# Kernel tuning notes

Measured on AMD Instinct MI355X. Metric: run time of the kernel, lower is better.

## Reference

```python
import jax, jax.numpy as jnp
import numpy as np

EPS = 1e-08
SINKHORN_ITERS = 5
SINKHORN_TAU = 0.05


def l2_normalize(x, axis=-1):
    return x / (jnp.linalg.norm(x, axis=axis, keepdims=True) + EPS)


def sinkhorn_balanced(logits, iters=SINKHORN_ITERS, tau=SINKHORN_TAU):
    # logits: [B, N, K]
    b, n, k = logits.shape
    q = jnp.exp(logits / tau)
    q = q / (jnp.sum(q, axis=(1, 2), keepdims=True) + EPS)
    target_row = 1.0 / float(n)
    target_col = 1.0 / float(k)
    for _ in range(iters):
        q = q / (jnp.sum(q, axis=2, keepdims=True) + EPS) * target_row
        q = q / (jnp.sum(q, axis=1, keepdims=True) + EPS) * target_col
    q = q / (jnp.sum(q, axis=2, keepdims=True) + EPS)
    return q


def assign(x, proto):
    x_n = l2_normalize(x)          # [B,N,D]
    p_n = l2_normalize(proto)      # [K,D]
    sim = jnp.einsum('bnd,kd->bnk', x_n, p_n)
    a = sinkhorn_balanced(sim)
    z_rec = jnp.einsum('bnk,kd->bnd', a, p_n)
    return z_rec, a, sim


def setup_inputs() -> dict:
    key = jax.random.key(0)
    k1, k2, k3, k4 = jax.random.split(key, 4)
    B, N, D, K = 16, 1024, 256, 256
    return {
        'f_rgb': jax.random.normal(k1, (B, N, D), dtype=jnp.float32),
        'f_sn': jax.random.normal(k2, (B, N, D), dtype=jnp.float32),
        'proto_rgb': jax.random.normal(k3, (K, D), dtype=jnp.float32) * 0.02,
        'proto_sn': jax.random.normal(k4, (K, D), dtype=jnp.float32) * 0.02,
    }


def reference(f_rgb, f_sn, proto_rgb, proto_sn):
    z_rgb, assign_rgb, sim_rgb = assign(f_rgb, proto_rgb)
    z_sn, assign_sn, sim_sn = assign(f_sn, proto_sn)
    # cross-modal consistency maps: [B,N,N]
    rgb_to_sn = jnp.matmul(assign_rgb, jnp.swapaxes(assign_sn, -1, -2))
    sn_to_rgb = jnp.matmul(assign_sn, jnp.swapaxes(assign_rgb, -1, -2))
    sem_consistency = 0.5 * (
        1.0 - jnp.clip(jnp.mean(rgb_to_sn), 0.0, 1.0)
        + 1.0 - jnp.clip(jnp.mean(sn_to_rgb), 0.0, 1.0)
    )
    return (z_rgb, z_sn, assign_rgb, assign_sn, sim_rgb, sim_sn, sem_consistency)
```

## Files before the change

kernel.cpp:

```cpp
#include <hip/hip_runtime.h>
#include <hip/hip_bf16.h>
#include <cstdint>
#include <cstddef>

#define EPS 1e-8f

typedef __attribute__((ext_vector_type(8))) short short8;
typedef __attribute__((ext_vector_type(4))) float floatx4;

static constexpr int Bb = 16, Nn = 1024, Dd = 256, Kk = 256;
static constexpr int M = Bb * Nn;
static constexpr size_t PM = (size_t)M * 256;

static constexpr size_t OUT_Z      = 0;
static constexpr size_t OUT_ASSIGN = 2 * PM;
static constexpr size_t OUT_SIM    = 4 * PM;
static constexpr size_t OUT_SEM    = 6 * PM;

static constexpr size_t OFF_QB  = 16777216;
static constexpr size_t OFF_PN  = 33554432;
static constexpr size_t OFF_PNT = 33816576;
static constexpr size_t OFF_U   = 34078720;
static constexpr size_t OFF_T   = 34209792;
static constexpr size_t OFF_SC  = 34209920;
static constexpr size_t OFF_CS  = 34406528;
static constexpr size_t ZERO_OFF = OFF_T;
static constexpr size_t ZERO_SZ  = 128 + 196608 + 32768;
static constexpr int    NZ_FLOATS = (int)(ZERO_SZ / 4);

__device__ __forceinline__ unsigned short f2bf(float f) {
    unsigned int b = __float_as_uint(f);
    b += 0x7fffu + ((b >> 16) & 1u);
    return (unsigned short)(b >> 16);
}
__device__ __forceinline__ float bf2f(unsigned short u) {
    return __uint_as_float(((unsigned int)u) << 16);
}

typedef const __attribute__((address_space(1))) unsigned int* gas_u32p;
typedef __attribute__((address_space(3))) unsigned int* las_u32p;
__device__ __forceinline__ void lds_cp16(const unsigned short* g, short* l) {
    __builtin_amdgcn_global_load_lds((gas_u32p)g, (las_u32p)l, 16, 0, 0);
}

__global__ __launch_bounds__(64) void proto_kernel(const float* __restrict__ pr,
                                                   const float* __restrict__ ps,
                                                   unsigned short* __restrict__ pn,
                                                   unsigned short* __restrict__ pnt,
                                                   float* __restrict__ zp) {
    int gid = blockIdx.x * 64 + threadIdx.x;
    for (int i = gid; i < NZ_FLOATS; i += 32768) zp[i] = 0.f;

    int row = blockIdx.x & 255;
    int mod = blockIdx.x >> 8;
    const float* p = (mod ? ps : pr) + (size_t)row * 256;
    int lane = threadIdx.x;
    float4 v = ((const float4*)p)[lane];
    float ss = v.x * v.x + v.y * v.y + v.z * v.z + v.w * v.w;
    #pragma unroll
    for (int m = 1; m < 64; m <<= 1) ss += __shfl_xor(ss, m);
    float sc = 1.0f / (sqrtf(ss) + EPS);
    ushort4 u4;
    u4.x = f2bf(v.x * sc); u4.y = f2bf(v.y * sc);
    u4.z = f2bf(v.z * sc); u4.w = f2bf(v.w * sc);
    *(ushort4*)(pn + (size_t)mod * 65536 + (size_t)row * 256 + lane * 4) = u4;
    unsigned short* pt = pnt + (size_t)mod * 65536 + row;
    pt[(size_t)(lane * 4 + 0) * 256] = u4.x;
    pt[(size_t)(lane * 4 + 1) * 256] = u4.y;
    pt[(size_t)(lane * 4 + 2) * 256] = u4.z;
    pt[(size_t)(lane * 4 + 3) * 256] = u4.w;
}

__global__ __launch_bounds__(256) void gemm0_fused(const float* __restrict__ fr,
                                                   const float* __restrict__ fs,
                                                   const unsigned short* __restrict__ pn,
                                                   unsigned short* __restrict__ qb,
                                                   float* __restrict__ doutf,
                                                   float* __restrict__ Tg) {
    __shared__ __align__(16) char smem[81920];
    short* Afull = (short*)smem;
    short* Bl    = (short*)(smem + 65536);

    int bx = blockIdx.x, by = blockIdx.y, mod = blockIdx.z;
    int t = threadIdx.x, lane = t & 63, wv = t >> 6;
    int wrow = (wv >> 1) * 64, wcol = (wv & 1) * 64;
    int g = lane >> 4, ml = lane & 15;

    const float* F0 = (mod ? fs : fr) + (size_t)by * 128 * 256;
    const unsigned short* B0 = pn + (size_t)mod * 65536 + (size_t)bx * 128 * 256;

    for (int bs = 0; bs < 4; bs++) {
        int rbase = wv * 32 + bs * 8;
        float4 vv[8];
        #pragma unroll
        for (int i = 0; i < 8; i++)
            vv[i] = ((const float4*)(F0 + (size_t)(rbase + i) * 256))[lane];
        #pragma unroll
        for (int i = 0; i < 8; i++) {
            float ss = vv[i].x * vv[i].x + vv[i].y * vv[i].y
                     + vv[i].z * vv[i].z + vv[i].w * vv[i].w;
            #pragma unroll
            for (int m = 1; m < 64; m <<= 1) ss += __shfl_xor(ss, m);
            float sc = 1.0f / (sqrtf(ss) + EPS);
            ushort4 u4;
            u4.x = f2bf(vv[i].x * sc); u4.y = f2bf(vv[i].y * sc);
            u4.z = f2bf(vv[i].z * sc); u4.w = f2bf(vv[i].w * sc);
            int row = rbase + i;
            int off = row * 256 + (((lane >> 1) ^ (row & 7)) << 3) + ((lane & 1) << 2);
            *(ushort4*)&Afull[off] = u4;
        }
    }

    floatx4 acc[4][4];
    #pragma unroll
    for (int i = 0; i < 4; i++)
        #pragma unroll
        for (int j = 0; j < 4; j++) acc[i][j] = (floatx4){0.f, 0.f, 0.f, 0.f};

    for (int kh = 0; kh < 4; kh++) {
        #pragma unroll
        for (int i = 0; i < 4; i++) {
            int sI = i * 256 + t;
            int r = sI >> 3, cs = sI & 7;
            int cg = cs ^ (r & 7);
            size_t goff = (size_t)r * 256 + kh * 64 + cg * 8;
            lds_cp16(B0 + goff, &Bl[sI * 8]);
        }
        __syncthreads();
        #pragma unroll
        for (int ks = 0; ks < 2; ks++) {
            short8 af[4], bfr[4];
            int c = ks * 4 + g;
            int c8 = kh * 8 + c;
            #pragma unroll
            for (int mt = 0; mt < 4; mt++) {
                int row = wrow + mt * 16 + ml;
                af[mt] = *(const short8*)&Afull[row * 256 + ((c8 ^ (row & 7)) << 3)];
            }
            #pragma unroll
            for (int nt = 0; nt < 4; nt++) {
                int col = wcol + nt * 16 + ml;
                bfr[nt] = *(const short8*)&Bl[col * 64 + ((c ^ (col & 7)) << 3)];
            }
            #pragma unroll
            for (int mt = 0; mt < 4; mt++)
                #pragma unroll
                for (int nt = 0; nt < 4; nt++)
                    acc[mt][nt] = __builtin_amdgcn_mfma_f32_16x16x32_bf16(af[mt], bfr[nt], acc[mt][nt], 0, 0, 0);
        }
        __syncthreads();
    }

    int g4 = g << 2;
    float tsum = 0.f;
    #pragma unroll
    for (int mt = 0; mt < 4; mt++)
        #pragma unroll
        for (int nt = 0; nt < 4; nt++)
            #pragma unroll
            for (int reg = 0; reg < 4; reg++) {
                float s = acc[mt][nt][reg];
                int row = by * 128 + wrow + mt * 16 + g4 + reg;
                int col = bx * 128 + wcol + nt * 16 + ml;
                size_t idx = (size_t)row * 256 + col;
                doutf[OUT_SIM + (size_t)mod * PM + idx] = s;
                unsigned short eb = f2bf(__expf(s * 20.0f));
                qb[(size_t)mod * PM + idx] = eb;
                tsum += bf2f(eb);
            }
    #pragma unroll
    for (int mk = 1; mk < 64; mk <<= 1) tsum += __shfl_xor(tsum, mk);
    float* tred = (float*)(smem + 65536);
    if (lane == 0) tred[wv] = tsum;
    __syncthreads();
    if (t == 0) atomicAdd(&Tg[mod * 16 + (by >> 3)], tred[0] + tred[1] + tred[2] + tred[3]);
}

__global__ __launch_bounds__(256) void pass_kernel(const unsigned short* __restrict__ qbg,
                                                   float* __restrict__ u,
                                                   const float* __restrict__ Tg,
                                                   float* __restrict__ Sc,
                                                   int pass) {
    __shared__ float vcur[256];
    __shared__ float unl[32];
    __shared__ float wsum[4][256];
    int tile = blockIdx.x, b = blockIdx.y, mod = blockIdx.z;
    int t = threadIdx.x;
    {
        float v = 1.0f;
        for (int j = 1; j < pass; j++) {
            float sc = Sc[((size_t)(mod * 6 + j) * 16 + b) * 256 + t];
            v = v * (1.0f / 256.0f) / (v * sc + EPS);
        }
        vcur[t] = v;
    }
    __syncthreads();

    int r = t >> 3, q = t & 7;
    size_t row = (size_t)b * 1024 + tile * 32 + r;
    const unsigned short* qrow = qbg + ((size_t)mod * M + row) * 256;
    const short8* q8 = (const short8*)(qrow + q * 32);
    const float4* v4 = (const float4*)(vcur + q * 32);
    float sr = 0.f;
    #pragma unroll
    for (int i = 0; i < 4; i++) {
        short8 qv = q8[i];
        float4 va = v4[2 * i], vb = v4[2 * i + 1];
        sr += bf2f((unsigned short)qv[0]) * va.x + bf2f((unsigned short)qv[1]) * va.y
            + bf2f((unsigned short)qv[2]) * va.z + bf2f((unsigned short)qv[3]) * va.w
            + bf2f((unsigned short)qv[4]) * vb.x + bf2f((unsigned short)qv[5]) * vb.y
            + bf2f((unsigned short)qv[6]) * vb.z + bf2f((unsigned short)qv[7]) * vb.w;
    }
    sr += __shfl_xor(sr, 1);
    sr += __shfl_xor(sr, 2);
    sr += __shfl_xor(sr, 4);

    float up = (pass == 1) ? 1.0f / (Tg[mod * 16 + b] + EPS) : u[(size_t)mod * M + row];
    float un = up * (1.0f / 1024.0f) / (up * sr + EPS);
    if (q == 0) {
        u[(size_t)mod * M + row] = un;
        unl[r] = un;
    }
    __syncthreads();

    int wv = t >> 6, lane = t & 63;
    float c0 = 0.f, c1 = 0.f, c2 = 0.f, c3 = 0.f;
    size_t rowbase = (size_t)mod * M + (size_t)b * 1024 + tile * 32;
    #pragma unroll
    for (int rr8 = 0; rr8 < 8; rr8++) {
        int rr = wv * 8 + rr8;
        float unr = unl[rr];
        ushort4 qv = *(const ushort4*)(qbg + (rowbase + rr) * 256 + lane * 4);
        c0 += bf2f(qv.x) * unr;
        c1 += bf2f(qv.y) * unr;
        c2 += bf2f(qv.z) * unr;
        c3 += bf2f(qv.w) * unr;
    }
    *(float4*)&wsum[wv][lane * 4] = make_float4(c0, c1, c2, c3);
    __syncthreads();
    {
        float ssum = wsum[0][t] + wsum[1][t] + wsum[2][t] + wsum[3][t];
        atomicAdd(&Sc[((size_t)(mod * 6 + pass) * 16 + b) * 256 + t], ssum);
    }
}

__global__ __launch_bounds__(256) void gemm1_fused(const unsigned short* __restrict__ qbg,
                                                   const unsigned short* __restrict__ pnt,
                                                   const float* __restrict__ u,
                                                   const float* __restrict__ Sc,
                                                   float* __restrict__ cs,
                                                   float* __restrict__ doutf) {
    __shared__ __align__(16) char smem[81920];
    short* Afull = (short*)smem;
    short* Bl    = (short*)(smem + 65536);
    float* vl    = (float*)(smem + 65536);
    float* unl   = (float*)(smem + 65536 + 1024);
    float* wsum  = (float*)(smem + 65536 + 2048);

    int bx = blockIdx.x, by = blockIdx.y, mod = blockIdx.z;
    int b = by >> 3;
    int t = threadIdx.x, lane = t & 63, wv = t >> 6;
    int wrow = (wv >> 1) * 64, wcol = (wv & 1) * 64;
    int g = lane >> 4, ml = lane & 15;
    int r = t >> 3, q = t & 7;
    size_t rowg0 = (size_t)by * 128;

    if (t < 256) {
        float v = 1.0f;
        #pragma unroll
        for (int j = 1; j <= 5; j++) {
            float scv = Sc[((size_t)(mod * 6 + j) * 16 + b) * 256 + t];
            v = v * (1.0f / 256.0f) / (v * scv + EPS);
        }
        vl[t] = v;
    }
    __syncthreads();

    const float* vb0 = vl + q * 32;
    for (int s = 0; s < 4; s++) {
        int rl = s * 32 + r;
        size_t rowg = rowg0 + rl;
        const short8* q8 = (const short8*)(qbg + ((size_t)mod * PM + rowg * 256) + q * 32);
        float sr = 0.f;
        #pragma unroll
        for (int i = 0; i < 4; i++) {
            short8 qv = q8[i];
            float4 va = *(const float4*)(vb0 + i * 8);
            float4 vb = *(const float4*)(vb0 + i * 8 + 4);
            sr += bf2f((unsigned short)qv[0]) * va.x + bf2f((unsigned short)qv[1]) * va.y
                + bf2f((unsigned short)qv[2]) * va.z + bf2f((unsigned short)qv[3]) * va.w
                + bf2f((unsigned short)qv[4]) * vb.x + bf2f((unsigned short)qv[5]) * vb.y
                + bf2f((unsigned short)qv[6]) * vb.z + bf2f((unsigned short)qv[7]) * vb.w;
        }
        sr += __shfl_xor(sr, 1);
        sr += __shfl_xor(sr, 2);
        sr += __shfl_xor(sr, 4);
        float up = u[(size_t)mod * M + rowg];
        float un = up / (up * sr + EPS);
        if (q == 0) unl[rl] = un;
    }
    __syncthreads();

    {
        float c0 = 0.f, c1 = 0.f, c2 = 0.f, c3 = 0.f;
        float4 vv = *(const float4*)(vl + lane * 4);
        float* aout = doutf + OUT_ASSIGN + (size_t)mod * PM;
        for (int s = 0; s < 4; s++) {
            #pragma unroll
            for (int k = 0; k < 8; k++) {
                int rl = s * 32 + wv * 8 + k;
                size_t rowg = rowg0 + rl;
                float unr = unl[rl];
                ushort4 qv = *(const ushort4*)(qbg + ((size_t)mod * PM + rowg * 256) + lane * 4);
                float4 a = make_float4(bf2f(qv.x) * unr * vv.x, bf2f(qv.y) * unr * vv.y,
                                       bf2f(qv.z) * unr * vv.z, bf2f(qv.w) * unr * vv.w);
                if (bx == 0) *(float4*)(aout + rowg * 256 + lane * 4) = a;
                ushort4 o;
                o.x = f2bf(a.x); o.y = f2bf(a.y); o.z = f2bf(a.z); o.w = f2bf(a.w);
                int off = rl * 256 + (((lane >> 1) ^ (rl & 7)) << 3) + ((lane & 1) << 2);
                *(ushort4*)&Afull[off] = o;
                c0 += a.x; c1 += a.y; c2 += a.z; c3 += a.w;
            }
        }
        *(float4*)&wsum[wv * 256 + lane * 4] = make_float4(c0, c1, c2, c3);
    }
    __syncthreads();
    if (bx == 0 && t < 256) {
        float ssum = wsum[0 * 256 + t] + wsum[1 * 256 + t] + wsum[2 * 256 + t] + wsum[3 * 256 + t];
        atomicAdd(&cs[((size_t)mod * 16 + b) * 256 + t], ssum);
    }
    __syncthreads();

    const unsigned short* B0 = pnt + (size_t)mod * 65536 + (size_t)bx * 128 * 256;
    floatx4 acc[4][4];
    #pragma unroll
    for (int i = 0; i < 4; i++)
        #pragma unroll
        for (int j = 0; j < 4; j++) acc[i][j] = (floatx4){0.f, 0.f, 0.f, 0.f};

    for (int kh = 0; kh < 4; kh++) {
        #pragma unroll
        for (int i = 0; i < 4; i++) {
            int sI = i * 256 + t;
            int rr = sI >> 3, cc = sI & 7;
            int cg = cc ^ (rr & 7);
            size_t goff = (size_t)rr * 256 + kh * 64 + cg * 8;
            lds_cp16(B0 + goff, &Bl[sI * 8]);
        }
        __syncthreads();
        #pragma unroll
        for (int ks = 0; ks < 2; ks++) {
            short8 af[4], bfr[4];
            int c = ks * 4 + g;
            int c8 = kh * 8 + c;
            #pragma unroll
            for (int mt = 0; mt < 4; mt++) {
                int row = wrow + mt * 16 + ml;
                af[mt] = *(const short8*)&Afull[row * 256 + ((c8 ^ (row & 7)) << 3)];
            }
            #pragma unroll
            for (int nt = 0; nt < 4; nt++) {
                int col = wcol + nt * 16 + ml;
                bfr[nt] = *(const short8*)&Bl[col * 64 + ((c ^ (col & 7)) << 3)];
            }
            #pragma unroll
            for (int mt = 0; mt < 4; mt++)
                #pragma unroll
                for (int nt = 0; nt < 4; nt++)
                    acc[mt][nt] = __builtin_amdgcn_mfma_f32_16x16x32_bf16(af[mt], bfr[nt], acc[mt][nt], 0, 0, 0);
        }
        __syncthreads();
    }

    int g4 = g << 2;
    float* dst = doutf + OUT_Z + (size_t)mod * PM;
    #pragma unroll
    for (int mt = 0; mt < 4; mt++)
        #pragma unroll
        for (int nt = 0; nt < 4; nt++)
            #pragma unroll
            for (int reg = 0; reg < 4; reg++) {
                int row = by * 128 + wrow + mt * 16 + g4 + reg;
                int col = bx * 128 + wcol + nt * 16 + ml;
                dst[(size_t)row * 256 + col] = acc[mt][nt][reg];
            }
}

__global__ __launch_bounds__(256) void sem_kernel(const float* __restrict__ cs,
                                                  float* __restrict__ doutf) {
    int t = threadIdx.x;
    float s = 0.f;
    #pragma unroll
    for (int b = 0; b < 16; b++)
        s += cs[b * 256 + t] * cs[4096 + b * 256 + t];
    #pragma unroll
    for (int mk = 1; mk < 64; mk <<= 1) s += __shfl_xor(s, mk);
    __shared__ float red[4];
    if ((t & 63) == 0) red[t >> 6] = s;
    __syncthreads();
    if (t == 0) {
        float tot = red[0] + red[1] + red[2] + red[3];
        float mv = tot / 16777216.0f;
        mv = fminf(fmaxf(mv, 0.f), 1.f);
        doutf[OUT_SEM] = 1.0f - mv;
    }
}

extern "C" void kernel_launch(void* const* d_in, const int* in_sizes, int n_in,
                              void* d_out, int out_size, void* d_ws, size_t ws_size,
                              hipStream_t stream) {
    const float* f_rgb = (const float*)d_in[0];
    const float* f_sn  = (const float*)d_in[1];
    const float* p_rgb = (const float*)d_in[2];
    const float* p_sn  = (const float*)d_in[3];
    char* ws = (char*)d_ws;
    unsigned short* qb   = (unsigned short*)(ws + OFF_QB);
    unsigned short* pn   = (unsigned short*)(ws + OFF_PN);
    unsigned short* pnt  = (unsigned short*)(ws + OFF_PNT);
    float* u             = (float*)(ws + OFF_U);
    float* Tg            = (float*)(ws + OFF_T);
    float* Sc            = (float*)(ws + OFF_SC);
    float* cs            = (float*)(ws + OFF_CS);
    float* doutf         = (float*)d_out;

    proto_kernel<<<dim3(512), 64, 0, stream>>>(p_rgb, p_sn, pn, pnt, (float*)(ws + ZERO_OFF));
    gemm0_fused<<<dim3(2, 128, 2), 256, 0, stream>>>(f_rgb, f_sn, pn, qb, doutf, Tg);
    for (int p = 1; p <= 5; p++)
        pass_kernel<<<dim3(32, 16, 2), 256, 0, stream>>>(qb, u, Tg, Sc, p);
    gemm1_fused<<<dim3(2, 128, 2), 256, 0, stream>>>(qb, pnt, u, Sc, cs, doutf);
    sem_kernel<<<1, 256, 0, stream>>>(cs, doutf);
}
```

Measured before the change: 192.1 us.

## Fuse five Sinkhorn passes into one persistent kernel with grid barriers

Replaces five separate pass_kernel launches with a single persistent kernel. Each block now handles 64 rows and keeps the row scales u in shared memory across passes, writing them to global memory only after the last pass. A per-(mod,batch) atomic counter barrier synchronises the 16 tiles of each group between passes. This removes four launch gaps and the per-pass global u traffic, and the row tiles may stay cache-resident. In exchange, correctness depends on all 512 blocks being co-resident, since spin barriers can deadlock otherwise, and there is added barrier latency.

```diff
diff --git a/kernel.cpp b/kernel.cpp
--- a/kernel.cpp
+++ b/kernel.cpp
@@ -17,6 +17,7 @@
 static constexpr size_t OUT_SIM    = 4 * PM;
 static constexpr size_t OUT_SEM    = 6 * PM;
 
+static constexpr size_t OFF_BAR = 0;
 static constexpr size_t OFF_QB  = 16777216;
 static constexpr size_t OFF_PN  = 33554432;
 static constexpr size_t OFF_PNT = 33816576;
@@ -47,9 +48,11 @@
                                                    const float* __restrict__ ps,
                                                    unsigned short* __restrict__ pn,
                                                    unsigned short* __restrict__ pnt,
-                                                   float* __restrict__ zp) {
+                                                   float* __restrict__ zp,
+                                                   unsigned int* __restrict__ bar) {
     int gid = blockIdx.x * 64 + threadIdx.x;
     for (int i = gid; i < NZ_FLOATS; i += 32768) zp[i] = 0.f;
+    if (gid < 32) bar[gid] = 0u;
 
     int row = blockIdx.x & 255;
     int mod = blockIdx.x >> 8;
@@ -176,71 +179,89 @@
     if (t == 0) atomicAdd(&Tg[mod * 16 + (by >> 3)], tred[0] + tred[1] + tred[2] + tred[3]);
 }
 
-__global__ __launch_bounds__(256) void pass_kernel(const unsigned short* __restrict__ qbg,
-                                                   float* __restrict__ u,
-                                                   const float* __restrict__ Tg,
-                                                   float* __restrict__ Sc,
-                                                   int pass) {
+__global__ __launch_bounds__(256, 4) void sink5_kernel(const unsigned short* __restrict__ qbg,
+                                                       float* __restrict__ u,
+                                                       const float* __restrict__ Tg,
+                                                       float* __restrict__ Sc,
+                                                       unsigned int* __restrict__ bar) {
     __shared__ float vcur[256];
-    __shared__ float unl[32];
+    __shared__ float unl[64];
     __shared__ float wsum[4][256];
     int tile = blockIdx.x, b = blockIdx.y, mod = blockIdx.z;
     int t = threadIdx.x;
-    {
-        float v = 1.0f;
-        for (int j = 1; j < pass; j++) {
-            float sc = Sc[((size_t)(mod * 6 + j) * 16 + b) * 256 + t];
-            v = v * (1.0f / 256.0f) / (v * sc + EPS);
-        }
-        vcur[t] = v;
-    }
-    __syncthreads();
-
+    int wv = t >> 6, lane = t & 63;
     int r = t >> 3, q = t & 7;
-    size_t row = (size_t)b * 1024 + tile * 32 + r;
-    const unsigned short* qrow = qbg + ((size_t)mod * M + row) * 256;
-    const short8* q8 = (const short8*)(qrow + q * 32);
-    const float4* v4 = (const float4*)(vcur + q * 32);
-    float sr = 0.f;
-    #pragma unroll
-    for (int i = 0; i < 4; i++) {
-        short8 qv = q8[i];
-        float4 va = v4[2 * i], vb = v4[2 * i + 1];
-        sr += bf2f((unsigned short)qv[0]) * va.x + bf2f((unsigned short)qv[1]) * va.y
-            + bf2f((unsigned short)qv[2]) * va.z + bf2f((unsigned short)qv[3]) * va.w
-            + bf2f((unsigned short)qv[4]) * vb.x + bf2f((unsigned short)qv[5]) * vb.y
-            + bf2f((unsigned short)qv[6]) * vb.z + bf2f((unsigned short)qv[7]) * vb.w;
-    }
-    sr += __shfl_xor(sr, 1);
-    sr += __shfl_xor(sr, 2);
-    sr += __shfl_xor(sr, 4);
-
-    float up = (pass == 1) ? 1.0f / (Tg[mod * 16 + b] + EPS) : u[(size_t)mod * M + row];
-    float un = up * (1.0f / 1024.0f) / (up * sr + EPS);
-    if (q == 0) {
-        u[(size_t)mod * M + row] = un;
-        unl[r] = un;
-    }
-    __syncthreads();
-
-    int wv = t >> 6, lane = t & 63;
-    float c0 = 0.f, c1 = 0.f, c2 = 0.f, c3 = 0.f;
-    size_t rowbase = (size_t)mod * M + (size_t)b * 1024 + tile * 32;
-    #pragma unroll
-    for (int rr8 = 0; rr8 < 8; rr8++) {
-        int rr = wv * 8 + rr8;
-        float unr = unl[rr];
-        ushort4 qv = *(const ushort4*)(qbg + (rowbase + rr) * 256 + lane * 4);
-        c0 += bf2f(qv.x) * unr;
-        c1 += bf2f(qv.y) * unr;
-        c2 += bf2f(qv.z) * unr;
-        c3 += bf2f(qv.w) * unr;
-    }
-    *(float4*)&wsum[wv][lane * 4] = make_float4(c0, c1, c2, c3);
-    __syncthreads();
-    {
-        float ssum = wsum[0][t] + wsum[1][t] + wsum[2][t] + wsum[3][t];
-        atomicAdd(&Sc[((size_t)(mod * 6 + pass) * 16 + b) * 256 + t], ssum);
+    size_t rowbase = (size_t)b * 1024 + tile * 64;
+    const unsigned short* qbase = qbg + ((size_t)mod * M + rowbase) * 256;
+    float u0 = 1.0f / (Tg[mod * 16 + b] + EPS);
+    unsigned int* bp = bar + (mod * 16 + b);
+
+    for (int pass = 1; pass <= 5; pass++) {
+        if (pass == 1) {
+            vcur[t] = 1.0f;
+        } else {
+            float sc = __hip_atomic_load(&Sc[((size_t)(mod * 6 + pass - 1) * 16 + b) * 256 + t],
+                                         __ATOMIC_RELAXED, __HIP_MEMORY_SCOPE_AGENT);
+            float v = vcur[t];
+            vcur[t] = v * (1.0f / 256.0f) / (v * sc + EPS);
+        }
+        __syncthreads();
+
+        const float4* v4 = (const float4*)(vcur + q * 32);
+        #pragma unroll
+        for (int h = 0; h < 2; h++) {
+            int rr = r + h * 32;
+            const short8* q8 = (const short8*)(qbase + (size_t)rr * 256 + q * 32);
+            float sr = 0.f;
+            #pragma unroll
+            for (int i = 0; i < 4; i++) {
+                short8 qv = q8[i];
+                float4 va = v4[2 * i], vb = v4[2 * i + 1];
+                sr += bf2f((unsigned short)qv[0]) * va.x + bf2f((unsigned short)qv[1]) * va.y
+                    + bf2f((unsigned short)qv[2]) * va.z + bf2f((unsigned short)qv[3]) * va.w
+                    + bf2f((unsigned short)qv[4]) * vb.x + bf2f((unsigned short)qv[5]) * vb.y
+                    + bf2f((unsigned short)qv[6]) * vb.z + bf2f((unsigned short)qv[7]) * vb.w;
+            }
+            sr += __shfl_xor(sr, 1);
+            sr += __shfl_xor(sr, 2);
+            sr += __shfl_xor(sr, 4);
+            float up = (pass == 1) ? u0 : unl[rr];
+            float un = up * (1.0f / 1024.0f) / (up * sr + EPS);
+            if (q == 0) {
+                unl[rr] = un;
+                if (pass == 5) u[(size_t)mod * M + rowbase + rr] = un;
+            }
+        }
+        __syncthreads();
+
+        float c0 = 0.f, c1 = 0.f, c2 = 0.f, c3 = 0.f;
+        #pragma unroll
+        for (int k = 0; k < 16; k++) {
+            int rr = wv * 16 + k;
+            float unr = unl[rr];
+            ushort4 qv = *(const ushort4*)(qbase + (size_t)rr * 256 + lane * 4);
+            c0 += bf2f(qv.x) * unr;
+            c1 += bf2f(qv.y) * unr;
+            c2 += bf2f(qv.z) * unr;
+            c3 += bf2f(qv.w) * unr;
+        }
+        *(float4*)&wsum[wv][lane * 4] = make_float4(c0, c1, c2, c3);
+        __syncthreads();
+        {
+            float ssum = wsum[0][t] + wsum[1][t] + wsum[2][t] + wsum[3][t];
+            atomicAdd(&Sc[((size_t)(mod * 6 + pass) * 16 + b) * 256 + t], ssum);
+        }
+
+        if (pass < 5) {
+            __syncthreads();
+            if (t == 0) {
+                __hip_atomic_fetch_add(bp, 1u, __ATOMIC_RELEASE, __HIP_MEMORY_SCOPE_AGENT);
+                while (__hip_atomic_load(bp, __ATOMIC_ACQUIRE, __HIP_MEMORY_SCOPE_AGENT)
+                       < (unsigned)(pass * 16))
+                    __builtin_amdgcn_s_sleep(8);
+            }
+            __syncthreads();
+        }
     }
 }
 
@@ -414,6 +435,7 @@
     const float* p_rgb = (const float*)d_in[2];
     const float* p_sn  = (const float*)d_in[3];
     char* ws = (char*)d_ws;
+    unsigned int* bar    = (unsigned int*)(ws + OFF_BAR);
     unsigned short* qb   = (unsigned short*)(ws + OFF_QB);
     unsigned short* pn   = (unsigned short*)(ws + OFF_PN);
     unsigned short* pnt  = (unsigned short*)(ws + OFF_PNT);
@@ -423,10 +445,9 @@
     float* cs            = (float*)(ws + OFF_CS);
     float* doutf         = (float*)d_out;
 
-    proto_kernel<<<dim3(512), 64, 0, stream>>>(p_rgb, p_sn, pn, pnt, (float*)(ws + ZERO_OFF));
+    proto_kernel<<<dim3(512), 64, 0, stream>>>(p_rgb, p_sn, pn, pnt, (float*)(ws + ZERO_OFF), bar);
     gemm0_fused<<<dim3(2, 128, 2), 256, 0, stream>>>(f_rgb, f_sn, pn, qb, doutf, Tg);
-    for (int p = 1; p <= 5; p++)
-        pass_kernel<<<dim3(32, 16, 2), 256, 0, stream>>>(qb, u, Tg, Sc, p);
+    sink5_kernel<<<dim3(16, 16, 2), 256, 0, stream>>>(qb, u, Tg, Sc, bar);
     gemm1_fused<<<dim3(2, 128, 2), 256, 0, stream>>>(qb, pnt, u, Sc, cs, doutf);
     sem_kernel<<<1, 256, 0, stream>>>(cs, doutf);
 }
```

Result: slower. 347.8 us (+81.1%).
